# Kernel tuning notes

Measured on AMD Instinct MI355X. Metric: run time of the kernel, lower is better.

## Reference

```python
import jax, jax.numpy as jnp
import numpy as np

RADIUS = 0.1
NSAMPLE = 32


def setup_inputs() -> dict:
    key = jax.random.key(0)
    k1, k2, k3 = jax.random.split(key, 3)
    B, N, P, C = 2, 16384, 4096, 64
    xyz = jax.random.uniform(k1, (B, N, 3), dtype=jnp.float32)
    new_xyz = jax.random.uniform(k2, (B, P, 3), dtype=jnp.float32)
    features = jax.random.normal(k3, (B, C, N), dtype=jnp.float32)
    return {"xyz": xyz, "new_xyz": new_xyz, "features": features}


def _ball_query(xyz, new_xyz, radius, nsample):
    """Return (B, npoint, nsample) int32 indices of the first `nsample` points
    (in original order) within `radius` of each query center. Slots beyond the
    number of valid neighbors are padded with the first valid index (0 if none),
    matching the standard PointNet++ CUDA ball_query semantics."""
    N = xyz.shape[1]
    # squared distances [B, P, N]
    d2 = jnp.sum((new_xyz[:, :, None, :] - xyz[:, None, :, :]) ** 2, axis=-1)
    in_ball = d2 < (radius * radius)
    # score = point index if in ball, else N (sentinel); smallest nsample scores
    # are the first nsample in-ball indices in original order.
    score = jnp.where(in_ball, jnp.arange(N, dtype=jnp.int32), jnp.int32(N))
    neg_topk, _ = jax.lax.top_k(-score, nsample)  # largest of -score == smallest score
    idx = -neg_topk  # [B, P, nsample], ascending
    first = idx[..., :1]
    idx = jnp.where(idx >= N, first, idx)  # pad invalid slots with first valid
    idx = jnp.where(idx >= N, 0, idx)      # no neighbor at all -> 0
    return idx


def _group(features, idx):
    """features (B, C, N), idx (B, P, S) -> (B, C, P, S)"""
    return jax.vmap(lambda f, i: f[:, i])(features, idx)


def reference(xyz, new_xyz, features):
    idx = _ball_query(xyz, new_xyz, RADIUS, NSAMPLE)          # (B, P, S)
    xyz_t = jnp.transpose(xyz, (0, 2, 1))                      # (B, 3, N)
    grouped_xyz = _group(xyz_t, idx)                           # (B, 3, P, S)
    grouped_xyz = grouped_xyz - jnp.transpose(new_xyz, (0, 2, 1))[..., None]
    grouped_features = _group(features, idx)                   # (B, C, P, S)
    new_features = jnp.concatenate([grouped_xyz, grouped_features], axis=1)
    return new_features
```

## Files before the change

kernel.cpp:

```cpp
#include <hip/hip_runtime.h>
#include <limits.h>

#define BB 2
#define NN 16384
#define PP 4096
#define CC 64
#define SS 32
#define R2 0.01f
#define OUTCH (3 + CC)
#define GRES 10
#define NCELL 1000
#define TILE 128

__device__ __forceinline__ int cell_of(float v) {
  int q = (int)(v * 10.0f);
  return q < 0 ? 0 : (q > GRES - 1 ? GRES - 1 : q);
}
__device__ __forceinline__ int cell_clamp_floor(float v) {
  int q = (int)floorf(v * 10.0f);
  return q < 0 ? 0 : (q > GRES - 1 ? GRES - 1 : q);
}

__global__ __launch_bounds__(256) void hist_kernel(const float* __restrict__ xyz,
                                                   int* __restrict__ hist) {
  const int i = blockIdx.x * 256 + threadIdx.x;
  const int b = i >> 14;
  const float* p = xyz + (size_t)i * 3;
  const int c = (cell_of(p[2]) * GRES + cell_of(p[1])) * GRES + cell_of(p[0]);
  atomicAdd(hist + b * NCELL + c, 1);
}

__global__ __launch_bounds__(1024) void scan_kernel(const int* __restrict__ hist,
                                                    int* __restrict__ cellStart) {
  __shared__ int sm[1024];
  const int b = blockIdx.x;
  const int t = threadIdx.x;
  const int own = (t < NCELL) ? hist[b * NCELL + t] : 0;
  sm[t] = own;
  __syncthreads();
  for (int off = 1; off < 1024; off <<= 1) {
    const int v = (t >= off) ? sm[t - off] : 0;
    __syncthreads();
    sm[t] += v;
    __syncthreads();
  }
  if (t < NCELL) cellStart[b * 1001 + t] = sm[t] - own;
  if (t == NCELL - 1) cellStart[b * 1001 + NCELL] = sm[t];
}

__global__ __launch_bounds__(256) void scatter_kernel(
    const float* __restrict__ xyz, const int* __restrict__ cellStart,
    int* __restrict__ fill, float4* __restrict__ sorted4) {
  const int i = blockIdx.x * 256 + threadIdx.x;
  const int b = i >> 14;
  const float* p = xyz + (size_t)i * 3;
  const float x = p[0], y = p[1], z = p[2];
  const int c = (cell_of(z) * GRES + cell_of(y)) * GRES + cell_of(x);
  const int r = atomicAdd(fill + b * NCELL + c, 1);
  const int pos = cellStart[b * 1001 + c] + r;
  float4 v;
  v.x = x; v.y = y; v.z = z; v.w = __int_as_float(i & (NN - 1));
  sorted4[(size_t)b * NN + pos] = v;
}

__global__ __launch_bounds__(256) void transpose_feat_kernel(
    const float* __restrict__ feat, float* __restrict__ featT) {
  __shared__ float tile[64][65];
  const int n0 = blockIdx.x * 64;
  const int b = blockIdx.y;
  const int jn = threadIdx.x & 63;
  const int g4 = threadIdx.x >> 6;

  const float* fb = feat + (size_t)b * CC * NN;
#pragma unroll
  for (int k = 0; k < 16; ++k) {
    const int c = g4 * 16 + k;
    tile[c][jn] = fb[(size_t)c * NN + n0 + jn];
  }
  __syncthreads();
  float* ft = featT + ((size_t)b * NN + n0) * CC;
#pragma unroll
  for (int k = 0; k < 16; ++k) {
    const int j = g4 * 16 + k;
    ft[(size_t)j * CC + jn] = tile[jn][j];
  }
}

__global__ __launch_bounds__(256) void query_group_kernel(
    const float4* __restrict__ sorted4, const int* __restrict__ cellStart,
    const float* __restrict__ new_xyz, const float* __restrict__ xyz,
    const float* __restrict__ featT, float* __restrict__ out) {
#pragma clang fp contract(off)
  __shared__ float smem[TILE * 65];
  __shared__ int idxsm[TILE];
  const int widx = threadIdx.x >> 6;
  const int lane = threadIdx.x & 63;
  const int wave = blockIdx.x * 4 + widx;
  const int b = wave >> 12;
  unsigned* bm = (unsigned*)smem + widx * 576;
  int* myout = idxsm + widx * SS;

  const float cx = new_xyz[wave * 3 + 0];
  const float cy = new_xyz[wave * 3 + 1];
  const float cz = new_xyz[wave * 3 + 2];
  const float4* __restrict__ sb = sorted4 + (size_t)b * NN;
  const int* __restrict__ csb = cellStart + b * 1001;

#pragma unroll
  for (int k = 0; k < 9; ++k) bm[k * 64 + lane] = 0;

  const float mg = 0.1f + 1e-5f;
  const int loy = cell_clamp_floor(cy - mg), hiy = cell_clamp_floor(cy + mg);
  const int loz = cell_clamp_floor(cz - mg), hiz = cell_clamp_floor(cz + mg);
  const int ny = hiy - loy + 1;
  const int nz = hiz - loz + 1;
  const int nr = nz * ny;

  int s_l = 0, len_l = 0;
  if (lane < nr) {
    int zi, yi;
    if (ny == 1) { zi = lane; yi = 0; }
    else if (ny == 2) { zi = lane >> 1; yi = lane & 1; }
    else { zi = (lane * 11) >> 5; yi = lane - zi * 3; }
    const int zc = loz + zi, yc = loy + yi;
    const float y0 = yc * 0.1f, z0 = zc * 0.1f;
    const float dymin = fmaxf(fmaxf(y0 - cy, cy - (y0 + 0.1f)), 0.0f);
    const float dzmin = fmaxf(fmaxf(z0 - cz, cz - (z0 + 0.1f)), 0.0f);
    const float rem = mg * mg - dymin * dymin - dzmin * dzmin;
    if (rem > 0.0f) {
      const float dxa = sqrtf(rem) * 1.0000002f + 1e-7f;
      const int lxr = cell_clamp_floor(cx - dxa);
      const int hxr = cell_clamp_floor(cx + dxa);
      const int c0 = (zc * GRES + yc) * GRES + lxr;
      s_l = csb[c0];
      len_l = csb[c0 + (hxr - lxr + 1)] - s_l;
    }
  }
  int incl = len_l;
#pragma unroll
  for (int d = 1; d <= 8; d <<= 1) {
    const int v = __shfl_up(incl, d);
    if (lane >= d) incl += v;
  }
  const int T = __shfl(incl, nr - 1);
  const int Lx = incl - len_l;

  int Lk[9], Sk[9];
#pragma unroll
  for (int k = 0; k < 9; ++k) {
    Lk[k] = __shfl(Lx, k);
    Sk[k] = __shfl(s_l, k);
  }

  auto flat_load = [&](int g) -> float4 {
    int L = Lk[0], S = Sk[0];
#pragma unroll
    for (int k = 1; k < 9; ++k) {
      const bool cge = g >= Lk[k];
      L = cge ? Lk[k] : L;
      S = cge ? Sk[k] : S;
    }
    return sb[S + (g - L)];
  };

  const int nIt = (T + 63) >> 6;
  float4 cur = {};
  if (lane < T) cur = flat_load(lane);
  for (int it = 0; it < nIt; ++it) {
    float4 nxt = cur;
    const int gn = (it + 1) * 64 + lane;
    if (gn < T) nxt = flat_load(gn);
    const int g = it * 64 + lane;
    if (g < T) {
      const float dx = cx - cur.x;
      const float dy = cy - cur.y;
      const float dz = cz - cur.z;
      const float a = dx * dx + dy * dy;
      const float d2 = a + dz * dz;
      if (d2 < R2) {
        const int orig = __float_as_int(cur.w);
        const int wi = orig >> 5;
        atomicOr(&bm[(wi >> 3) * 9 + (wi & 7)], 1u << (orig & 31));
      }
    }
    cur = nxt;
  }
  __threadfence_block();

  unsigned wv[8];
  int c = 0;
  int fi = INT_MAX;
#pragma unroll
  for (int k = 0; k < 8; ++k) {
    wv[k] = bm[lane * 9 + k];
    c += (int)__popc(wv[k]);
    if (fi == INT_MAX && wv[k])
      fi = lane * 256 + k * 32 + (int)__builtin_ctz(wv[k]);
  }

  int incl2 = c;
#pragma unroll
  for (int d = 1; d < 64; d <<= 1) {
    const int t = __shfl_up(incl2, d);
    if (lane >= d) incl2 += t;
  }
  const int E = incl2 - c;
  const int total = __shfl(incl2, 63);

  const unsigned long long nb = __ballot(c > 0);
  int fc = 0;
  if (nb) fc = __shfl(fi, (int)__builtin_ctzll(nb));

  int s = E;
  if (s < SS) {
#pragma unroll
    for (int k = 0; k < 8; ++k) {
      unsigned ww = wv[k];
      while (ww && s < SS) {
        const int bpos = (int)__builtin_ctz(ww);
        ww &= ww - 1;
        myout[s++] = lane * 256 + k * 32 + bpos;
      }
      if (s >= SS) break;
    }
  }
  for (int s2 = total + lane; s2 < SS; s2 += 64) myout[s2] = fc;

  __syncthreads();

  const int base = blockIdx.x * TILE;
  const int t = threadIdx.x;
  const size_t PS = (size_t)PP * SS;

  const float4* ftb = (const float4*)(featT + (size_t)b * NN * CC);
#pragma unroll
  for (int k = 0; k < 8; ++k) {
    const int u = k * 256 + t;
    const int r = u >> 4;
    const int q = u & 15;
    const int v = idxsm[r];
    const float4 val = ftb[(size_t)v * 16 + q];
    float* dst = &smem[r * 65 + q * 4];
    dst[0] = val.x; dst[1] = val.y; dst[2] = val.z; dst[3] = val.w;
  }
  __syncthreads();

  if (t < TILE) {
    const int g = base + t;
    const int v = idxsm[t];
    const int p = (g >> 5) & (PP - 1);
    const float* xr = xyz + ((size_t)b * NN + v) * 3;
    const float* cr = new_xyz + (size_t)(b * PP + p) * 3;
    const size_t ob = (size_t)b * OUTCH * PS + ((size_t)g & (PS - 1));
    out[ob + 0 * PS] = xr[0] - cr[0];
    out[ob + 1 * PS] = xr[1] - cr[1];
    out[ob + 2 * PS] = xr[2] - cr[2];
  }

  float* ob3 = out + (size_t)b * OUTCH * PS + 3 * PS + ((size_t)base & (PS - 1));
#pragma unroll
  for (int k = 0; k < 32; ++k) {
    const int u = k * 256 + t;
    const int c2 = u >> 7;
    const int r = u & 127;
    ob3[(size_t)c2 * PS + r] = smem[r * 65 + c2];
  }
}

extern "C" void kernel_launch(void* const* d_in, const int* in_sizes, int n_in,
                              void* d_out, int out_size, void* d_ws, size_t ws_size,
                              hipStream_t stream) {
  const float* xyz = (const float*)d_in[0];
  const float* new_xyz = (const float*)d_in[1];
  const float* feat = (const float*)d_in[2];
  float* out = (float*)d_out;

  float* featT = (float*)d_ws;
  char* p = (char*)d_ws + (size_t)BB * NN * CC * sizeof(float);
  float4* sorted4 = (float4*)p;
  p += (size_t)BB * NN * sizeof(float4);
  int* cellStart = (int*)p;
  p += (size_t)BB * 1001 * sizeof(int);
  int* hist = (int*)p;
  int* fill = hist + BB * NCELL;

  hipMemsetAsync(hist, 0, (size_t)2 * BB * NCELL * sizeof(int), stream);
  hist_kernel<<<(BB * NN) / 256, 256, 0, stream>>>(xyz, hist);
  scan_kernel<<<BB, 1024, 0, stream>>>(hist, cellStart);
  scatter_kernel<<<(BB * NN) / 256, 256, 0, stream>>>(xyz, cellStart, fill, sorted4);
  transpose_feat_kernel<<<dim3(NN / 64, BB), 256, 0, stream>>>(feat, featT);
  query_group_kernel<<<(BB * PP) / 4, 256, 0, stream>>>(sorted4, cellStart,
                                                        new_xyz, xyz, featT, out);
}
```

Baseline: 66.27 us.

## Fuse histogram, scan and scatter into one grid-synced binning kernel

```diff
diff --git a/kernel.cpp b/kernel.cpp
--- a/kernel.cpp
+++ b/kernel.cpp
@@ -11,6 +11,7 @@
 #define GRES 10
 #define NCELL 1000
 #define TILE 128
+#define BINBLK 128
 
 __device__ __forceinline__ int cell_of(float v) {
   int q = (int)(v * 10.0f);
@@ -21,56 +22,19 @@
   return q < 0 ? 0 : (q > GRES - 1 ? GRES - 1 : q);
 }
 
-__global__ __launch_bounds__(256) void hist_kernel(const float* __restrict__ xyz,
-                                                   int* __restrict__ hist) {
-  const int i = blockIdx.x * 256 + threadIdx.x;
-  const int b = i >> 14;
-  const float* p = xyz + (size_t)i * 3;
-  const int c = (cell_of(p[2]) * GRES + cell_of(p[1])) * GRES + cell_of(p[0]);
-  atomicAdd(hist + b * NCELL + c, 1);
-}
-
-__global__ __launch_bounds__(1024) void scan_kernel(const int* __restrict__ hist,
-                                                    int* __restrict__ cellStart) {
-  __shared__ int sm[1024];
-  const int b = blockIdx.x;
-  const int t = threadIdx.x;
-  const int own = (t < NCELL) ? hist[b * NCELL + t] : 0;
-  sm[t] = own;
-  __syncthreads();
-  for (int off = 1; off < 1024; off <<= 1) {
-    const int v = (t >= off) ? sm[t - off] : 0;
-    __syncthreads();
-    sm[t] += v;
-    __syncthreads();
-  }
-  if (t < NCELL) cellStart[b * 1001 + t] = sm[t] - own;
-  if (t == NCELL - 1) cellStart[b * 1001 + NCELL] = sm[t];
-}
-
-__global__ __launch_bounds__(256) void scatter_kernel(
-    const float* __restrict__ xyz, const int* __restrict__ cellStart,
-    int* __restrict__ fill, float4* __restrict__ sorted4) {
-  const int i = blockIdx.x * 256 + threadIdx.x;
-  const int b = i >> 14;
-  const float* p = xyz + (size_t)i * 3;
-  const float x = p[0], y = p[1], z = p[2];
-  const int c = (cell_of(z) * GRES + cell_of(y)) * GRES + cell_of(x);
-  const int r = atomicAdd(fill + b * NCELL + c, 1);
-  const int pos = cellStart[b * 1001 + c] + r;
-  float4 v;
-  v.x = x; v.y = y; v.z = z; v.w = __int_as_float(i & (NN - 1));
-  sorted4[(size_t)b * NN + pos] = v;
-}
-
 __global__ __launch_bounds__(256) void transpose_feat_kernel(
-    const float* __restrict__ feat, float* __restrict__ featT) {
+    const float* __restrict__ feat, float* __restrict__ featT,
+    int* __restrict__ zeroRegion) {
   __shared__ float tile[64][65];
   const int n0 = blockIdx.x * 64;
   const int b = blockIdx.y;
   const int jn = threadIdx.x & 63;
   const int g4 = threadIdx.x >> 6;
 
+  if (blockIdx.x == 0 && blockIdx.y == 0) {
+    for (int k = threadIdx.x; k < 2 * BB * NCELL + 8; k += 256) zeroRegion[k] = 0;
+  }
+
   const float* fb = feat + (size_t)b * CC * NN;
 #pragma unroll
   for (int k = 0; k < 16; ++k) {
@@ -84,6 +48,79 @@
     const int j = g4 * 16 + k;
     ft[(size_t)j * CC + jn] = tile[jn][j];
   }
+}
+
+__global__ __launch_bounds__(256) void bin_all_kernel(
+    const float* __restrict__ xyz, int* __restrict__ histG,
+    int* __restrict__ fillG, int* __restrict__ doneG,
+    int* __restrict__ cellStartG, float4* __restrict__ sorted4) {
+  __shared__ int cstart[NCELL];
+  __shared__ int wsum[4];
+  const int blk = blockIdx.x;
+  const int b = blk >> 6;
+  const int t = threadIdx.x;
+  const int lane = t & 63;
+  const int w = t >> 6;
+  const int i = (blk & 63) * 256 + t;
+
+  const float* p = xyz + ((size_t)b * NN + i) * 3;
+  const float x = p[0], y = p[1], z = p[2];
+  const int c = (cell_of(z) * GRES + cell_of(y)) * GRES + cell_of(x);
+  atomicAdd(histG + b * NCELL + c, 1);
+
+  __threadfence();
+  __syncthreads();
+  if (t == 0) {
+    atomicAdd(doneG, 1);
+    while (__hip_atomic_load(doneG, __ATOMIC_ACQUIRE,
+                             __HIP_MEMORY_SCOPE_AGENT) < BINBLK) {
+    }
+  }
+  __syncthreads();
+
+  int v0 = 0, v1 = 0, v2 = 0, v3 = 0, s = 0;
+  if (t < 250) {
+    const int base = b * NCELL + t * 4;
+    v0 = __hip_atomic_load(histG + base + 0, __ATOMIC_RELAXED, __HIP_MEMORY_SCOPE_AGENT);
+    v1 = __hip_atomic_load(histG + base + 1, __ATOMIC_RELAXED, __HIP_MEMORY_SCOPE_AGENT);
+    v2 = __hip_atomic_load(histG + base + 2, __ATOMIC_RELAXED, __HIP_MEMORY_SCOPE_AGENT);
+    v3 = __hip_atomic_load(histG + base + 3, __ATOMIC_RELAXED, __HIP_MEMORY_SCOPE_AGENT);
+    s = v0 + v1 + v2 + v3;
+  }
+  int incl = s;
+#pragma unroll
+  for (int d = 1; d < 64; d <<= 1) {
+    const int u = __shfl_up(incl, d);
+    if (lane >= d) incl += u;
+  }
+  if (lane == 63) wsum[w] = incl;
+  __syncthreads();
+  int pre = 0;
+#pragma unroll
+  for (int k = 0; k < 4; ++k) pre += (k < w) ? wsum[k] : 0;
+  if (t < 250) {
+    int run = pre + incl - s;
+    cstart[t * 4 + 0] = run; run += v0;
+    cstart[t * 4 + 1] = run; run += v1;
+    cstart[t * 4 + 2] = run; run += v2;
+    cstart[t * 4 + 3] = run;
+  }
+  __syncthreads();
+
+  if ((blk & 63) == 0) {
+    if (t < 250) {
+#pragma unroll
+      for (int k = 0; k < 4; ++k)
+        cellStartG[b * 1001 + t * 4 + k] = cstart[t * 4 + k];
+    }
+    if (t == 0) cellStartG[b * 1001 + NCELL] = NN;
+  }
+
+  const int r = atomicAdd(fillG + b * NCELL + c, 1);
+  const int pos = cstart[c] + r;
+  float4 vv;
+  vv.x = x; vv.y = y; vv.z = z; vv.w = __int_as_float(i);
+  sorted4[(size_t)b * NN + pos] = vv;
 }
 
 __global__ __launch_bounds__(256) void query_group_kernel(
@@ -283,12 +320,11 @@
   p += (size_t)BB * 1001 * sizeof(int);
   int* hist = (int*)p;
   int* fill = hist + BB * NCELL;
-
-  hipMemsetAsync(hist, 0, (size_t)2 * BB * NCELL * sizeof(int), stream);
-  hist_kernel<<<(BB * NN) / 256, 256, 0, stream>>>(xyz, hist);
-  scan_kernel<<<BB, 1024, 0, stream>>>(hist, cellStart);
-  scatter_kernel<<<(BB * NN) / 256, 256, 0, stream>>>(xyz, cellStart, fill, sorted4);
-  transpose_feat_kernel<<<dim3(NN / 64, BB), 256, 0, stream>>>(feat, featT);
+  int* done = fill + BB * NCELL;
+
+  transpose_feat_kernel<<<dim3(NN / 64, BB), 256, 0, stream>>>(feat, featT, hist);
+  bin_all_kernel<<<BINBLK, 256, 0, stream>>>(xyz, hist, fill, done, cellStart,
+                                             sorted4);
   query_group_kernel<<<(BB * PP) / 4, 256, 0, stream>>>(sorted4, cellStart,
                                                         new_xyz, xyz, featT, out);
 }
```

Result: faster. 64.07 us (-3.3%).

## Split query and grouping kernels, fold memset into transpose, use shuffle scan

Applied to the files above, without the earlier changes.

```diff
diff --git a/kernel.cpp b/kernel.cpp
--- a/kernel.cpp
+++ b/kernel.cpp
@@ -21,6 +21,34 @@
   return q < 0 ? 0 : (q > GRES - 1 ? GRES - 1 : q);
 }
 
+__global__ __launch_bounds__(256) void transpose_feat_kernel(
+    const float* __restrict__ feat, float* __restrict__ featT,
+    int* __restrict__ zeroRegion) {
+  __shared__ float tile[64][65];
+  const int n0 = blockIdx.x * 64;
+  const int b = blockIdx.y;
+  const int jn = threadIdx.x & 63;
+  const int g4 = threadIdx.x >> 6;
+
+  if (blockIdx.x == 0 && blockIdx.y == 0) {
+    for (int k = threadIdx.x; k < 2 * BB * NCELL + 8; k += 256) zeroRegion[k] = 0;
+  }
+
+  const float* fb = feat + (size_t)b * CC * NN;
+#pragma unroll
+  for (int k = 0; k < 16; ++k) {
+    const int c = g4 * 16 + k;
+    tile[c][jn] = fb[(size_t)c * NN + n0 + jn];
+  }
+  __syncthreads();
+  float* ft = featT + ((size_t)b * NN + n0) * CC;
+#pragma unroll
+  for (int k = 0; k < 16; ++k) {
+    const int j = g4 * 16 + k;
+    ft[(size_t)j * CC + jn] = tile[jn][j];
+  }
+}
+
 __global__ __launch_bounds__(256) void hist_kernel(const float* __restrict__ xyz,
                                                    int* __restrict__ hist) {
   const int i = blockIdx.x * 256 + threadIdx.x;
@@ -30,26 +58,46 @@
   atomicAdd(hist + b * NCELL + c, 1);
 }
 
-__global__ __launch_bounds__(1024) void scan_kernel(const int* __restrict__ hist,
-                                                    int* __restrict__ cellStart) {
-  __shared__ int sm[1024];
+__global__ __launch_bounds__(256) void scan_fast_kernel(
+    const int* __restrict__ hist, int* __restrict__ cellStartG) {
+  __shared__ int wsum[4];
   const int b = blockIdx.x;
   const int t = threadIdx.x;
-  const int own = (t < NCELL) ? hist[b * NCELL + t] : 0;
-  sm[t] = own;
+  const int lane = t & 63;
+  const int w = t >> 6;
+
+  int v0 = 0, v1 = 0, v2 = 0, v3 = 0, s = 0;
+  if (t < 250) {
+    const int base = b * NCELL + t * 4;
+    v0 = hist[base + 0];
+    v1 = hist[base + 1];
+    v2 = hist[base + 2];
+    v3 = hist[base + 3];
+    s = v0 + v1 + v2 + v3;
+  }
+  int incl = s;
+#pragma unroll
+  for (int d = 1; d < 64; d <<= 1) {
+    const int u = __shfl_up(incl, d);
+    if (lane >= d) incl += u;
+  }
+  if (lane == 63) wsum[w] = incl;
   __syncthreads();
-  for (int off = 1; off < 1024; off <<= 1) {
-    const int v = (t >= off) ? sm[t - off] : 0;
-    __syncthreads();
-    sm[t] += v;
-    __syncthreads();
-  }
-  if (t < NCELL) cellStart[b * 1001 + t] = sm[t] - own;
-  if (t == NCELL - 1) cellStart[b * 1001 + NCELL] = sm[t];
+  int pre = 0;
+#pragma unroll
+  for (int k = 0; k < 4; ++k) pre += (k < w) ? wsum[k] : 0;
+  if (t < 250) {
+    int run = pre + incl - s;
+    cellStartG[b * 1001 + t * 4 + 0] = run; run += v0;
+    cellStartG[b * 1001 + t * 4 + 1] = run; run += v1;
+    cellStartG[b * 1001 + t * 4 + 2] = run; run += v2;
+    cellStartG[b * 1001 + t * 4 + 3] = run;
+  }
+  if (t == 0) cellStartG[b * 1001 + NCELL] = NN;
 }
 
 __global__ __launch_bounds__(256) void scatter_kernel(
-    const float* __restrict__ xyz, const int* __restrict__ cellStart,
+    const float* __restrict__ xyz, const int* __restrict__ cellStartG,
     int* __restrict__ fill, float4* __restrict__ sorted4) {
   const int i = blockIdx.x * 256 + threadIdx.x;
   const int b = i >> 14;
@@ -57,48 +105,23 @@
   const float x = p[0], y = p[1], z = p[2];
   const int c = (cell_of(z) * GRES + cell_of(y)) * GRES + cell_of(x);
   const int r = atomicAdd(fill + b * NCELL + c, 1);
-  const int pos = cellStart[b * 1001 + c] + r;
+  const int pos = cellStartG[b * 1001 + c] + r;
   float4 v;
   v.x = x; v.y = y; v.z = z; v.w = __int_as_float(i & (NN - 1));
   sorted4[(size_t)b * NN + pos] = v;
 }
 
-__global__ __launch_bounds__(256) void transpose_feat_kernel(
-    const float* __restrict__ feat, float* __restrict__ featT) {
-  __shared__ float tile[64][65];
-  const int n0 = blockIdx.x * 64;
-  const int b = blockIdx.y;
-  const int jn = threadIdx.x & 63;
-  const int g4 = threadIdx.x >> 6;
-
-  const float* fb = feat + (size_t)b * CC * NN;
-#pragma unroll
-  for (int k = 0; k < 16; ++k) {
-    const int c = g4 * 16 + k;
-    tile[c][jn] = fb[(size_t)c * NN + n0 + jn];
-  }
-  __syncthreads();
-  float* ft = featT + ((size_t)b * NN + n0) * CC;
-#pragma unroll
-  for (int k = 0; k < 16; ++k) {
-    const int j = g4 * 16 + k;
-    ft[(size_t)j * CC + jn] = tile[jn][j];
-  }
-}
-
-__global__ __launch_bounds__(256) void query_group_kernel(
+__global__ __launch_bounds__(256) void ball_query_kernel(
     const float4* __restrict__ sorted4, const int* __restrict__ cellStart,
-    const float* __restrict__ new_xyz, const float* __restrict__ xyz,
-    const float* __restrict__ featT, float* __restrict__ out) {
+    const float* __restrict__ new_xyz, ushort* __restrict__ idxU) {
 #pragma clang fp contract(off)
-  __shared__ float smem[TILE * 65];
-  __shared__ int idxsm[TILE];
+  __shared__ unsigned bmAll[4 * 576];
   const int widx = threadIdx.x >> 6;
   const int lane = threadIdx.x & 63;
   const int wave = blockIdx.x * 4 + widx;
   const int b = wave >> 12;
-  unsigned* bm = (unsigned*)smem + widx * 576;
-  int* myout = idxsm + widx * SS;
+  unsigned* bm = bmAll + widx * 576;
+  ushort* myout = idxU + wave * SS;
 
   const float cx = new_xyz[wave * 3 + 0];
   const float cy = new_xyz[wave * 3 + 1];
@@ -219,18 +242,27 @@
       while (ww && s < SS) {
         const int bpos = (int)__builtin_ctz(ww);
         ww &= ww - 1;
-        myout[s++] = lane * 256 + k * 32 + bpos;
+        myout[s++] = (ushort)(lane * 256 + k * 32 + bpos);
       }
       if (s >= SS) break;
     }
   }
-  for (int s2 = total + lane; s2 < SS; s2 += 64) myout[s2] = fc;
-
-  __syncthreads();
-
+  for (int s2 = total + lane; s2 < SS; s2 += 64) myout[s2] = (ushort)fc;
+}
+
+__global__ __launch_bounds__(256) void group_kernel_t(
+    const float* __restrict__ xyz, const float* __restrict__ new_xyz,
+    const float* __restrict__ featT, const ushort* __restrict__ idxU,
+    float* __restrict__ out) {
+  __shared__ float lds[TILE * 65];
+  __shared__ int idxsm[TILE];
   const int base = blockIdx.x * TILE;
+  const int b = base >> 17;
   const int t = threadIdx.x;
   const size_t PS = (size_t)PP * SS;
+
+  if (t < TILE) idxsm[t] = (int)idxU[base + t];
+  __syncthreads();
 
   const float4* ftb = (const float4*)(featT + (size_t)b * NN * CC);
 #pragma unroll
@@ -240,7 +272,7 @@
     const int q = u & 15;
     const int v = idxsm[r];
     const float4 val = ftb[(size_t)v * 16 + q];
-    float* dst = &smem[r * 65 + q * 4];
+    float* dst = &lds[r * 65 + q * 4];
     dst[0] = val.x; dst[1] = val.y; dst[2] = val.z; dst[3] = val.w;
   }
   __syncthreads();
@@ -263,7 +295,7 @@
     const int u = k * 256 + t;
     const int c2 = u >> 7;
     const int r = u & 127;
-    ob3[(size_t)c2 * PS + r] = smem[r * 65 + c2];
+    ob3[(size_t)c2 * PS + r] = lds[r * 65 + c2];
   }
 }
 
@@ -279,16 +311,19 @@
   char* p = (char*)d_ws + (size_t)BB * NN * CC * sizeof(float);
   float4* sorted4 = (float4*)p;
   p += (size_t)BB * NN * sizeof(float4);
+  ushort* idxU = (ushort*)p;
+  p += (size_t)BB * PP * SS * sizeof(ushort);
   int* cellStart = (int*)p;
   p += (size_t)BB * 1001 * sizeof(int);
   int* hist = (int*)p;
   int* fill = hist + BB * NCELL;
 
-  hipMemsetAsync(hist, 0, (size_t)2 * BB * NCELL * sizeof(int), stream);
+  transpose_feat_kernel<<<dim3(NN / 64, BB), 256, 0, stream>>>(feat, featT, hist);
   hist_kernel<<<(BB * NN) / 256, 256, 0, stream>>>(xyz, hist);
-  scan_kernel<<<BB, 1024, 0, stream>>>(hist, cellStart);
+  scan_fast_kernel<<<BB, 256, 0, stream>>>(hist, cellStart);
   scatter_kernel<<<(BB * NN) / 256, 256, 0, stream>>>(xyz, cellStart, fill, sorted4);
-  transpose_feat_kernel<<<dim3(NN / 64, BB), 256, 0, stream>>>(feat, featT);
-  query_group_kernel<<<(BB * PP) / 4, 256, 0, stream>>>(sorted4, cellStart,
-                                                        new_xyz, xyz, featT, out);
-}
+  ball_query_kernel<<<(BB * PP) / 4, 256, 0, stream>>>(sorted4, cellStart,
+                                                       new_xyz, idxU);
+  group_kernel_t<<<(BB * PP * SS) / TILE, 256, 0, stream>>>(xyz, new_xyz, featT,
+                                                            idxU, out);
+}
```

Result: slower. 82.96 us (+25.2%).
